# Optimization experiments

Measured on AMD Instinct MI355X. Metric: run time of the kernel, lower is better.

## Reference

```python
import jax, jax.numpy as jnp
import numpy as np

EPS = 1e-5
ROPE_BASE = 10000.0
N_HEAD = 16


def rms_norm(x, eps=EPS):
    return x * jax.lax.rsqrt(jnp.mean(x * x, axis=-1, keepdims=True) + eps)


def rope(x):
    # x: [B, H, L, D]; non-standard interleaved variant from the source:
    # x_odd = x[..., 1::2], x_even = x[..., ::2]
    # y = interleave(y_odd, y_even)
    B, H, L, D = x.shape
    inv_freq = 1.0 / (ROPE_BASE ** (jnp.arange(0, D, 2, dtype=jnp.float32) / D))
    angles = jnp.arange(L, dtype=jnp.float32)[:, None] * inv_freq[None, :]  # [L, D/2]
    cos, sin = jnp.cos(angles), jnp.sin(angles)
    x_odd = x[..., 1::2].astype(jnp.float32)
    x_even = x[..., ::2].astype(jnp.float32)
    y_odd = x_odd * cos - x_even * sin
    y_even = x_odd * sin + x_even * cos
    y = jnp.stack([y_odd, y_even], axis=-1).reshape(B, H, L, D)
    return y.astype(x.dtype)


def setup_inputs() -> dict:
    key = jax.random.key(0)
    k1, k2, k3 = jax.random.split(key, 3)
    B, L, HID = 2, 2048, 2048
    in_std = 0.5 * HID ** (-0.5)
    bound = (3 ** 0.5) * in_std
    x = jax.random.normal(k1, (B, L, HID), dtype=jnp.float32)
    W_qkv = jax.random.uniform(k2, (3 * HID, HID), minval=-bound, maxval=bound, dtype=jnp.float32)
    # out_proj is zero-initialized in the source; use small random weights so the
    # output (and gradients) are non-trivial for correctness checking.
    W_out = jax.random.uniform(k3, (HID, HID), minval=-bound, maxval=bound, dtype=jnp.float32)
    return {"x": x, "W_qkv": W_qkv, "W_out": W_out}


def reference(x, W_qkv, W_out):
    B, L, HID = x.shape
    D = HID // N_HEAD
    qkv = jnp.einsum('blc,fc->blf', x, W_qkv)  # [B, L, 3*HID]
    q, k, v = jnp.split(qkv, 3, axis=-1)
    def heads(t):
        return t.reshape(B, L, N_HEAD, D).transpose(0, 2, 1, 3)  # [B,H,L,D]
    q, k, v = heads(q), heads(k), heads(v)
    q = rope(rms_norm(q))
    k = rope(rms_norm(k))
    scale = 1.0 / jnp.sqrt(jnp.asarray(D, dtype=jnp.float32))
    scores = jnp.einsum('bhqd,bhkd->bhqk', q, k) * scale
    causal = jnp.tril(jnp.ones((L, L), dtype=bool))
    scores = jnp.where(causal, scores, -jnp.inf)
    attn = jax.nn.softmax(scores, axis=-1)
    out = jnp.einsum('bhqk,bhkd->bhqd', attn, v)
    out = out.transpose(0, 2, 1, 3).reshape(B, L, HID)
    return jnp.einsum('blc,fc->blf', out, W_out)
```

## Files before the change

kernel.cpp:

```cpp
#include <hip/hip_runtime.h>
#include <stdint.h>
#include <math.h>

typedef unsigned short u16;
typedef unsigned int u32;
typedef __attribute__((ext_vector_type(8))) short bf16x8;
typedef __attribute__((ext_vector_type(4))) float f32x4;

#define SEQ 2048
#define HID 2048
#define NH  16
#define DH  128
#define NB  2

typedef __attribute__((address_space(1))) const u32 gu32;
typedef __attribute__((address_space(3))) u32 lu32;

__device__ __forceinline__ u16 f2bf(float f) {
  u32 u = __float_as_uint(f);
  return (u16)((u + 0x7fffu + ((u >> 16) & 1u)) >> 16);
}
__device__ __forceinline__ float bf2f(u16 h) { return __uint_as_float(((u32)h) << 16); }

__device__ __forceinline__ void gload_lds16(const void* g, void* l) {
  __builtin_amdgcn_global_load_lds((gu32*)g, (lu32*)l, 16, 0, 0);
}

__global__ __launch_bounds__(256) void k_cvt(const float* __restrict__ src, u16* __restrict__ dst, int n4) {
  int i = blockIdx.x * 256 + threadIdx.x;
  int stride = gridDim.x * 256;
  for (; i < n4; i += stride) {
    float4 v = ((const float4*)src)[i];
    ushort4 o;
    o.x = f2bf(v.x); o.y = f2bf(v.y); o.z = f2bf(v.z); o.w = f2bf(v.w);
    ((ushort4*)dst)[i] = o;
  }
}

template<int EPI>
__global__ __launch_bounds__(256)
void k_gemm(const u16* __restrict__ A, const u16* __restrict__ Bm,
            float* __restrict__ Cf, u16* __restrict__ Qr, u16* __restrict__ Kr, u16* __restrict__ Vr,
            int N, int K, int NX) {
  __shared__ alignas(16) char sA[128 * 128];
  __shared__ alignas(16) char sB[128 * 128];
  const int tid = threadIdx.x;
  const int wid = tid >> 6, lane = tid & 63;
  const int l15 = lane & 15, l4 = lane >> 4;
  const int nwg = gridDim.x, bid = blockIdx.x;
  const int wg = (bid & 7) * (nwg >> 3) + (bid >> 3);
  const int bx = wg % NX, by = wg / NX;
  const int m0 = by * 128, n0 = bx * 128;
  const int wr = (wid >> 1) * 64, wc = (wid & 1) * 64;

  f32x4 acc[4][4];
  #pragma unroll
  for (int i = 0; i < 4; ++i)
    #pragma unroll
    for (int j = 0; j < 4; ++j)
      acc[i][j] = (f32x4){0.f, 0.f, 0.f, 0.f};

  const int nkt = K >> 6;
  for (int kt = 0; kt < nkt; ++kt) {
    const int k0 = kt << 6;
    __syncthreads();
    #pragma unroll
    for (int it = 0; it < 4; ++it) {
      int o = it * 4096 + tid * 16;
      int row = o >> 7, cb = o & 127;
      int scb = cb ^ ((row & 7) << 4);
      gload_lds16((const char*)A + ((size_t)(m0 + row) * K + k0) * 2 + scb, &sA[it * 4096 + wid * 1024]);
    }
    #pragma unroll
    for (int it = 0; it < 4; ++it) {
      int o = it * 4096 + tid * 16;
      int row = o >> 7, cb = o & 127;
      int scb = cb ^ ((row & 7) << 4);
      gload_lds16((const char*)Bm + ((size_t)(n0 + row) * K + k0) * 2 + scb, &sB[it * 4096 + wid * 1024]);
    }
    __syncthreads();
    #pragma unroll
    for (int kk = 0; kk < 2; ++kk) {
      bf16x8 av[4], bv[4];
      #pragma unroll
      for (int mi = 0; mi < 4; ++mi) {
        int row = wr + mi * 16 + l15;
        int colb = kk * 64 + 16 * l4;
        av[mi] = *(const bf16x8*)&sA[row * 128 + (colb ^ ((row & 7) << 4))];
      }
      #pragma unroll
      for (int ni = 0; ni < 4; ++ni) {
        int row = wc + ni * 16 + l15;
        int colb = kk * 64 + 16 * l4;
        bv[ni] = *(const bf16x8*)&sB[row * 128 + (colb ^ ((row & 7) << 4))];
      }
      #pragma unroll
      for (int mi = 0; mi < 4; ++mi)
        #pragma unroll
        for (int ni = 0; ni < 4; ++ni)
          acc[mi][ni] = __builtin_amdgcn_mfma_f32_16x16x32_bf16(av[mi], bv[ni], acc[mi][ni], 0, 0, 0);
    }
  }

  #pragma unroll
  for (int mi = 0; mi < 4; ++mi) {
    #pragma unroll
    for (int ni = 0; ni < 4; ++ni) {
      #pragma unroll
      for (int j = 0; j < 4; ++j) {
        int gm = m0 + wr + mi * 16 + l4 * 4 + j;
        int gn = n0 + wc + ni * 16 + l15;
        float v = acc[mi][ni][j];
        if (EPI == 0) {
          int b = gm >> 11, l = gm & 2047;
          int which = gn >> 11, hid = gn & 2047;
          int h = hid >> 7, d = hid & 127;
          u16* dst = (which == 0) ? Qr : ((which == 1) ? Kr : Vr);
          size_t idx = ((size_t)(b * NH + h) * SEQ + l) * DH + d;
          dst[idx] = f2bf(v);
        } else {
          Cf[(size_t)gm * N + gn] = v;
        }
      }
    }
  }
}

__global__ __launch_bounds__(256) void k_vtr(const u16* __restrict__ Vr, u16* __restrict__ Vt) {
  __shared__ u16 tile[64][72];
  const int k0 = blockIdx.x * 64, d0 = blockIdx.y * 64, bh = blockIdx.z;
  const u16* src = Vr + ((size_t)bh << 18);
  u16* dst = Vt + ((size_t)bh << 18);
  const int tid = threadIdx.x;
  #pragma unroll
  for (int it = 0; it < 2; ++it) {
    int e = it * 2048 + tid * 8;
    int r = e >> 6, c = e & 63;
    bf16x8 v = *(const bf16x8*)(src + (size_t)(k0 + r) * DH + d0 + c);
    *(bf16x8*)&tile[r][c] = v;
  }
  __syncthreads();
  #pragma unroll
  for (int it = 0; it < 2; ++it) {
    int e = it * 2048 + tid * 8;
    int rd = e >> 6, ck = e & 63;
    bf16x8 w;
    #pragma unroll
    for (int i = 0; i < 8; ++i) w[i] = (short)tile[ck + i][rd];
    *(bf16x8*)(dst + (size_t)(d0 + rd) * SEQ + k0 + ck) = w;
  }
}

__global__ __launch_bounds__(256) void k_nrope(u16* __restrict__ T, float mul) {
  const int r = blockIdx.x * 4 + (threadIdx.x >> 6);
  const int lane = threadIdx.x & 63;
  u16* p = T + ((size_t)r << 7) + lane * 2;
  u32 pr = *(const u32*)p;
  float xe = bf2f((u16)(pr & 0xffffu));
  float xo = bf2f((u16)(pr >> 16));
  float ss = xe * xe + xo * xo;
  #pragma unroll
  for (int off = 1; off < 64; off <<= 1) ss += __shfl_xor(ss, off);
  float rinv = rsqrtf(ss * (1.f / 128.f) + 1e-5f);
  float e = xe * rinv, o = xo * rinv;
  int pos = r & (SEQ - 1);
  float freq = exp2f(-0.20762050593046014f * (float)lane);
  float ang = (float)pos * freq;
  float sn, cs;
  sincosf(ang, &sn, &cs);
  u32 outw = (u32)f2bf((o * cs - e * sn) * mul) | ((u32)f2bf((o * sn + e * cs) * mul) << 16);
  *(u32*)p = outw;
}

#define PSTR 72

__device__ __forceinline__ void attn_tile(const char* sK, const char* sVt, char* sPw,
                                          const bf16x8* aq, f32x4* accO, float& m_, float& se,
                                          int qpos, int kb, bool diag, int l15, int l4) {
  f32x4 sacc[4];
  __builtin_amdgcn_s_setprio(1);
  #pragma unroll
  for (int sj = 0; sj < 4; ++sj) {
    sacc[sj] = (f32x4){0.f, 0.f, 0.f, 0.f};
    int row = sj * 16 + l15;
    #pragma unroll
    for (int kk = 0; kk < 4; ++kk) {
      int colb = kk * 64 + 16 * l4;
      bf16x8 bk = *(const bf16x8*)&sK[(row << 8) + (colb ^ ((row & 7) << 4))];
      sacc[sj] = __builtin_amdgcn_mfma_f32_16x16x32_bf16(bk, aq[kk], sacc[sj], 0, 0, 0);
    }
  }
  __builtin_amdgcn_s_setprio(0);
  float pvv[16];
  float mx = -1e30f;
  #pragma unroll
  for (int sj = 0; sj < 4; ++sj)
    #pragma unroll
    for (int j = 0; j < 4; ++j) {
      float s = sacc[sj][j];
      if (diag) {
        int kpos = kb + sj * 16 + l4 * 4 + j;
        s = (kpos > qpos) ? -1e30f : s;
      }
      pvv[sj * 4 + j] = s;
      mx = fmaxf(mx, s);
    }
  mx = fmaxf(mx, __shfl_xor(mx, 16));
  mx = fmaxf(mx, __shfl_xor(mx, 32));
  float mn = fmaxf(m_, mx);
  float corr = __expf(m_ - mn);
  m_ = mn;
  float sum = 0.f;
  #pragma unroll
  for (int i = 0; i < 16; ++i) { float pe = __expf(pvv[i] - mn); pvv[i] = pe; sum += pe; }
  sum += __shfl_xor(sum, 16);
  sum += __shfl_xor(sum, 32);
  se = se * corr + sum;
  float corr4[4];
  #pragma unroll
  for (int j = 0; j < 4; ++j) corr4[j] = __shfl(corr, l4 * 4 + j);
  #pragma unroll
  for (int db = 0; db < 8; ++db) {
    f32x4 a = accO[db];
    #pragma unroll
    for (int j = 0; j < 4; ++j) a[j] *= corr4[j];
    accO[db] = a;
  }
  u16* Pw = (u16*)sPw;
  #pragma unroll
  for (int sj = 0; sj < 4; ++sj)
    #pragma unroll
    for (int jp = 0; jp < 2; ++jp) {
      u32 w = (u32)f2bf(pvv[sj * 4 + jp * 2]) | ((u32)f2bf(pvv[sj * 4 + jp * 2 + 1]) << 16);
      *(u32*)&Pw[l15 * PSTR + sj * 16 + l4 * 4 + jp * 2] = w;
    }
  bf16x8 pa0 = *(const bf16x8*)(sPw + l15 * (PSTR * 2) + 16 * l4);
  bf16x8 pa1 = *(const bf16x8*)(sPw + l15 * (PSTR * 2) + 16 * l4 + 64);
  __builtin_amdgcn_s_setprio(1);
  #pragma unroll
  for (int db = 0; db < 8; ++db) {
    int row = db * 16 + l15;
    const char* vb = &sVt[row * 128];
    bf16x8 b0 = *(const bf16x8*)&vb[(16 * l4) ^ ((row & 7) << 4)];
    bf16x8 b1 = *(const bf16x8*)&vb[(64 + 16 * l4) ^ ((row & 7) << 4)];
    accO[db] = __builtin_amdgcn_mfma_f32_16x16x32_bf16(pa0, b0, accO[db], 0, 0, 0);
    accO[db] = __builtin_amdgcn_mfma_f32_16x16x32_bf16(pa1, b1, accO[db], 0, 0, 0);
  }
  __builtin_amdgcn_s_setprio(0);
}

__device__ __forceinline__ void stage_kv(const char* Kp, const char* Vtp, int kb,
                                         char* bK, char* bV, int tid, int wid) {
  #pragma unroll
  for (int it = 0; it < 4; ++it) {
    int o = it * 4096 + tid * 16;
    int row = o >> 8, cb = o & 255;
    int scb = cb ^ ((row & 7) << 4);
    gload_lds16(Kp + (size_t)(kb + row) * 256 + scb, &bK[it * 4096 + wid * 1024]);
  }
  #pragma unroll
  for (int it = 0; it < 4; ++it) {
    int o = it * 4096 + tid * 16;
    int row = o >> 7, cb = o & 127;
    int scb = cb ^ ((row & 7) << 4);
    gload_lds16(Vtp + (size_t)row * (SEQ * 2) + kb * 2 + scb, &bV[it * 4096 + wid * 1024]);
  }
}

__global__ __launch_bounds__(256, 2)
void k_attn(const u16* __restrict__ Q, const u16* __restrict__ Kg,
            const u16* __restrict__ Vt, u16* __restrict__ O) {
  __shared__ alignas(16) char sK0[64 * 256];
  __shared__ alignas(16) char sK1[64 * 256];
  __shared__ alignas(16) char sV0[128 * 128];
  __shared__ alignas(16) char sV1[128 * 128];
  __shared__ alignas(16) char sP[4 * 16 * PSTR * 2];
  const int tid = threadIdx.x, wid = tid >> 6, lane = tid & 63;
  const int l15 = lane & 15, l4 = lane >> 4;
  const int i = blockIdx.x;
  const int xcd = i & 7, slot = i >> 3;
  const int p = slot & 15;
  const int bh = xcd + 8 * (slot >> 4);
  const int b = bh >> 4, h = bh & 15;
  const int tA = p, tB = 31 - p;
  const u16* Qp = Q + ((size_t)bh << 18);
  const char* Kp = (const char*)(Kg + ((size_t)bh << 18));
  const char* Vtp = (const char*)(Vt + ((size_t)bh << 18));
  const int q0A = tA * 64 + wid * 16;
  const int q0B = tB * 64 + wid * 16;

  bf16x8 aqA[4], aqB[4];
  #pragma unroll
  for (int kk = 0; kk < 4; ++kk) {
    aqA[kk] = *(const bf16x8*)(Qp + (size_t)(q0A + l15) * DH + kk * 32 + 8 * l4);
    aqB[kk] = *(const bf16x8*)(Qp + (size_t)(q0B + l15) * DH + kk * 32 + 8 * l4);
  }

  f32x4 accA[8], accB[8];
  #pragma unroll
  for (int i2 = 0; i2 < 8; ++i2) { accA[i2] = (f32x4){0.f,0.f,0.f,0.f}; accB[i2] = (f32x4){0.f,0.f,0.f,0.f}; }
  float mA = -1e30f, mB = -1e30f, seA = 0.f, seB = 0.f;

  char* sPw = sP + wid * (16 * PSTR * 2);
  const int nt = tB + 1;

  stage_kv(Kp, Vtp, 0, sK0, sV0, tid, wid);
  for (int t = 0; t < nt; ++t) {
    char* bK = (t & 1) ? sK1 : sK0;
    char* bV = (t & 1) ? sV1 : sV0;
    if (t + 1 < nt) {
      stage_kv(Kp, Vtp, (t + 1) << 6, (t & 1) ? sK0 : sK1, (t & 1) ? sV0 : sV1, tid, wid);
      asm volatile("s_waitcnt vmcnt(8)" ::: "memory");
    } else {
      asm volatile("s_waitcnt vmcnt(0)" ::: "memory");
    }
    __builtin_amdgcn_sched_barrier(0);
    __builtin_amdgcn_s_barrier();

    const int kb = t << 6;
    attn_tile(bK, bV, sPw, aqB, accB, mB, seB, q0B + l15, kb, t == tB, l15, l4);
    if (t <= tA)
      attn_tile(bK, bV, sPw, aqA, accA, mA, seA, q0A + l15, kb, t == tA, l15, l4);

    __builtin_amdgcn_s_barrier();
  }

  float seA4[4], seB4[4];
  #pragma unroll
  for (int j = 0; j < 4; ++j) {
    seA4[j] = __shfl(seA, l4 * 4 + j);
    seB4[j] = __shfl(seB, l4 * 4 + j);
  }
  #pragma unroll
  for (int db = 0; db < 8; ++db) {
    #pragma unroll
    for (int j = 0; j < 4; ++j) {
      int d = db * 16 + l15;
      int qA = q0A + l4 * 4 + j;
      int qB = q0B + l4 * 4 + j;
      O[(size_t)(b * SEQ + qA) * HID + h * DH + d] = f2bf(accA[db][j] / seA4[j]);
      O[(size_t)(b * SEQ + qB) * HID + h * DH + d] = f2bf(accB[db][j] / seB4[j]);
    }
  }
}

extern "C" void kernel_launch(void* const* d_in, const int* in_sizes, int n_in,
                              void* d_out, int out_size, void* d_ws, size_t ws_size,
                              hipStream_t stream) {
  (void)in_sizes; (void)n_in; (void)out_size; (void)ws_size;
  const float* x = (const float*)d_in[0];
  const float* Wqkv = (const float*)d_in[1];
  const float* Wout = (const float*)d_in[2];
  float* out = (float*)d_out;
  char* ws = (char*)d_ws;

  u16* xb  = (u16*)(ws);
  u16* wqb = (u16*)(ws + (size_t)16777216);
  u16* Vt  = wqb;
  u16* wob = (u16*)(ws + (size_t)16777216 + 25165824);
  u16* Qr  = (u16*)(ws + (size_t)50331648);
  u16* Kr  = Qr + (size_t)8388608;
  u16* Vr  = Kr + (size_t)8388608;
  u16* Ob  = xb;

  k_cvt<<<dim3(1024), dim3(256), 0, stream>>>(x, xb, (NB * SEQ * HID) / 4);
  k_cvt<<<dim3(1024), dim3(256), 0, stream>>>(Wqkv, wqb, (3 * HID * HID) / 4);
  k_cvt<<<dim3(1024), dim3(256), 0, stream>>>(Wout, wob, (HID * HID) / 4);

  k_gemm<0><<<dim3(1536), dim3(256), 0, stream>>>(xb, wqb, nullptr, Qr, Kr, Vr, 3 * HID, HID, 48);

  k_vtr<<<dim3(SEQ / 64, DH / 64, NB * NH), dim3(256), 0, stream>>>(Vr, Vt);
  k_nrope<<<dim3((NB * NH * SEQ) / 4), dim3(256), 0, stream>>>(Qr, 0.08838834764831845f);
  k_nrope<<<dim3((NB * NH * SEQ) / 4), dim3(256), 0, stream>>>(Kr, 1.0f);

  k_attn<<<dim3(512), dim3(256), 0, stream>>>(Qr, Kr, Vt, Ob);

  k_gemm<1><<<dim3(512), dim3(256), 0, stream>>>(Ob, wob, out, nullptr, nullptr, nullptr, HID, HID, 16);
}
```

Baseline: 301.8 us.

## Merge conversion and rope launches; interleave dual-tile attention with lazy rescale

The three fp32-to-bf16 conversion kernels are merged into one launch, and the two norm+rope launches become a single 2D-grid launch. In attention, the log2(e) factor is folded into the Q scale so exp2 replaces exp. When both query tiles are active, their QK^T and PV MFMAs are interleaved so each K/V fragment is loaded from LDS once. The softmax rescale of the accumulators is skipped unless the running max rises by more than 8, and the P scratch buffer uses an XOR swizzle instead of padding. The aim is fewer launches, less LDS traffic and fewer VALU ops, at the cost of higher register pressure and a threshold-based rescale that trades exactness of the max tracking for fewer multiplies.

After: 298.8 us (median of 3 runs). No clear change (-1.0%).

```diff
diff --git a/kernel.cpp b/kernel.cpp
--- a/kernel.cpp
+++ b/kernel.cpp
@@ -26,14 +26,21 @@
   __builtin_amdgcn_global_load_lds((gu32*)g, (lu32*)l, 16, 0, 0);
 }
 
-__global__ __launch_bounds__(256) void k_cvt(const float* __restrict__ src, u16* __restrict__ dst, int n4) {
+__global__ __launch_bounds__(256) void k_cvt3(const float* __restrict__ s0, u16* __restrict__ d0, int n0,
+                                              const float* __restrict__ s1, u16* __restrict__ d1, int n1,
+                                              const float* __restrict__ s2, u16* __restrict__ d2, int n2) {
   int i = blockIdx.x * 256 + threadIdx.x;
   int stride = gridDim.x * 256;
-  for (; i < n4; i += stride) {
-    float4 v = ((const float4*)src)[i];
+  int total = n0 + n1 + n2;
+  for (; i < total; i += stride) {
+    const float* s; u16* d; int k = i;
+    if (k < n0) { s = s0; d = d0; }
+    else if (k < n0 + n1) { s = s1; d = d1; k -= n0; }
+    else { s = s2; d = d2; k -= n0 + n1; }
+    float4 v = ((const float4*)s)[k];
     ushort4 o;
     o.x = f2bf(v.x); o.y = f2bf(v.y); o.z = f2bf(v.z); o.w = f2bf(v.w);
-    ((ushort4*)dst)[i] = o;
+    ((ushort4*)d)[k] = o;
   }
 }
 
@@ -151,7 +158,9 @@
   }
 }
 
-__global__ __launch_bounds__(256) void k_nrope(u16* __restrict__ T, float mul) {
+__global__ __launch_bounds__(256) void k_nrope2(u16* __restrict__ Qr, u16* __restrict__ Kr, float mq) {
+  u16* T = blockIdx.y ? Kr : Qr;
+  const float mul = blockIdx.y ? 1.0f : mq;
   const int r = blockIdx.x * 4 + (threadIdx.x >> 6);
   const int lane = threadIdx.x & 63;
   u16* p = T + ((size_t)r << 7) + lane * 2;
@@ -172,81 +181,65 @@
   *(u32*)p = outw;
 }
 
-#define PSTR 72
-
-__device__ __forceinline__ void attn_tile(const char* sK, const char* sVt, char* sPw,
-                                          const bf16x8* aq, f32x4* accO, float& m_, float& se,
-                                          int qpos, int kb, bool diag, int l15, int l4) {
-  f32x4 sacc[4];
-  __builtin_amdgcn_s_setprio(1);
-  #pragma unroll
-  for (int sj = 0; sj < 4; ++sj) {
-    sacc[sj] = (f32x4){0.f, 0.f, 0.f, 0.f};
-    int row = sj * 16 + l15;
-    #pragma unroll
-    for (int kk = 0; kk < 4; ++kk) {
-      int colb = kk * 64 + 16 * l4;
-      bf16x8 bk = *(const bf16x8*)&sK[(row << 8) + (colb ^ ((row & 7) << 4))];
-      sacc[sj] = __builtin_amdgcn_mfma_f32_16x16x32_bf16(bk, aq[kk], sacc[sj], 0, 0, 0);
-    }
-  }
-  __builtin_amdgcn_s_setprio(0);
-  float pvv[16];
-  float mx = -1e30f;
+
+__device__ __forceinline__ void smax(f32x4 (&sacc)[4], float& m_, float& se,
+                                     f32x4* accO, u32 (&pw)[8],
+                                     bool diag, int qpos, int kb, int l15, int l4) {
+  if (diag) {
+    #pragma unroll
+    for (int sj = 0; sj < 4; ++sj)
+      #pragma unroll
+      for (int j = 0; j < 4; ++j) {
+        int kpos = kb + sj * 16 + l4 * 4 + j;
+        if (kpos > qpos) sacc[sj][j] = -1e30f;
+      }
+  }
+  float mx = sacc[0][0];
   #pragma unroll
   for (int sj = 0; sj < 4; ++sj)
     #pragma unroll
-    for (int j = 0; j < 4; ++j) {
-      float s = sacc[sj][j];
-      if (diag) {
-        int kpos = kb + sj * 16 + l4 * 4 + j;
-        s = (kpos > qpos) ? -1e30f : s;
-      }
-      pvv[sj * 4 + j] = s;
-      mx = fmaxf(mx, s);
-    }
+    for (int j = 0; j < 4; ++j) mx = fmaxf(mx, sacc[sj][j]);
   mx = fmaxf(mx, __shfl_xor(mx, 16));
   mx = fmaxf(mx, __shfl_xor(mx, 32));
-  float mn = fmaxf(m_, mx);
-  float corr = __expf(m_ - mn);
-  m_ = mn;
+  if (!__all(mx <= m_ + 8.f)) {
+    float mn = fmaxf(m_, mx);
+    float corr = __builtin_exp2f(m_ - mn);
+    m_ = mn;
+    se *= corr;
+    float corr4[4];
+    #pragma unroll
+    for (int j = 0; j < 4; ++j) corr4[j] = __shfl(corr, l4 * 4 + j);
+    #pragma unroll
+    for (int db = 0; db < 8; ++db) {
+      f32x4 a = accO[db];
+      #pragma unroll
+      for (int j = 0; j < 4; ++j) a[j] *= corr4[j];
+      accO[db] = a;
+    }
+  }
   float sum = 0.f;
   #pragma unroll
-  for (int i = 0; i < 16; ++i) { float pe = __expf(pvv[i] - mn); pvv[i] = pe; sum += pe; }
+  for (int sj = 0; sj < 4; ++sj)
+    #pragma unroll
+    for (int jp = 0; jp < 2; ++jp) {
+      float p0 = __builtin_exp2f(sacc[sj][jp * 2]     - m_);
+      float p1 = __builtin_exp2f(sacc[sj][jp * 2 + 1] - m_);
+      pw[sj * 2 + jp] = (u32)f2bf(p0) | ((u32)f2bf(p1) << 16);
+      sum += p0 + p1;
+    }
   sum += __shfl_xor(sum, 16);
   sum += __shfl_xor(sum, 32);
-  se = se * corr + sum;
-  float corr4[4];
-  #pragma unroll
-  for (int j = 0; j < 4; ++j) corr4[j] = __shfl(corr, l4 * 4 + j);
-  #pragma unroll
-  for (int db = 0; db < 8; ++db) {
-    f32x4 a = accO[db];
-    #pragma unroll
-    for (int j = 0; j < 4; ++j) a[j] *= corr4[j];
-    accO[db] = a;
-  }
-  u16* Pw = (u16*)sPw;
+  se += sum;
+}
+
+__device__ __forceinline__ void pwrite(char* sPw, const u32 (&pw)[8], int l15, int l4) {
+  const int sw = (l15 & 7) << 4;
+  char* base = sPw + l15 * 128;
   #pragma unroll
   for (int sj = 0; sj < 4; ++sj)
     #pragma unroll
-    for (int jp = 0; jp < 2; ++jp) {
-      u32 w = (u32)f2bf(pvv[sj * 4 + jp * 2]) | ((u32)f2bf(pvv[sj * 4 + jp * 2 + 1]) << 16);
-      *(u32*)&Pw[l15 * PSTR + sj * 16 + l4 * 4 + jp * 2] = w;
-    }
-  bf16x8 pa0 = *(const bf16x8*)(sPw + l15 * (PSTR * 2) + 16 * l4);
-  bf16x8 pa1 = *(const bf16x8*)(sPw + l15 * (PSTR * 2) + 16 * l4 + 64);
-  __builtin_amdgcn_s_setprio(1);
-  #pragma unroll
-  for (int db = 0; db < 8; ++db) {
-    int row = db * 16 + l15;
-    const char* vb = &sVt[row * 128];
-    bf16x8 b0 = *(const bf16x8*)&vb[(16 * l4) ^ ((row & 7) << 4)];
-    bf16x8 b1 = *(const bf16x8*)&vb[(64 + 16 * l4) ^ ((row & 7) << 4)];
-    accO[db] = __builtin_amdgcn_mfma_f32_16x16x32_bf16(pa0, b0, accO[db], 0, 0, 0);
-    accO[db] = __builtin_amdgcn_mfma_f32_16x16x32_bf16(pa1, b1, accO[db], 0, 0, 0);
-  }
-  __builtin_amdgcn_s_setprio(0);
+    for (int jp = 0; jp < 2; ++jp)
+      *(u32*)(base + ((sj * 32 + l4 * 8 + jp * 4) ^ sw)) = pw[sj * 2 + jp];
 }
 
 __device__ __forceinline__ void stage_kv(const char* Kp, const char* Vtp, int kb,
@@ -274,7 +267,7 @@
   __shared__ alignas(16) char sK1[64 * 256];
   __shared__ alignas(16) char sV0[128 * 128];
   __shared__ alignas(16) char sV1[128 * 128];
-  __shared__ alignas(16) char sP[4 * 16 * PSTR * 2];
+  __shared__ alignas(16) char sP[4 * 2048];
   const int tid = threadIdx.x, wid = tid >> 6, lane = tid & 63;
   const int l15 = lane & 15, l4 = lane >> 4;
   const int i = blockIdx.x;
@@ -301,7 +294,8 @@
   for (int i2 = 0; i2 < 8; ++i2) { accA[i2] = (f32x4){0.f,0.f,0.f,0.f}; accB[i2] = (f32x4){0.f,0.f,0.f,0.f}; }
   float mA = -1e30f, mB = -1e30f, seA = 0.f, seB = 0.f;
 
-  char* sPw = sP + wid * (16 * PSTR * 2);
+  char* sPw = sP + wid * 2048;
+  const int psw = (l15 & 7) << 4;
   const int nt = tB + 1;
 
   stage_kv(Kp, Vtp, 0, sK0, sV0, tid, wid);
@@ -318,9 +312,81 @@
     __builtin_amdgcn_s_barrier();
 
     const int kb = t << 6;
-    attn_tile(bK, bV, sPw, aqB, accB, mB, seB, q0B + l15, kb, t == tB, l15, l4);
-    if (t <= tA)
-      attn_tile(bK, bV, sPw, aqA, accA, mA, seA, q0A + l15, kb, t == tA, l15, l4);
+    if (t <= tA) {
+      f32x4 sb[4], sa[4];
+      __builtin_amdgcn_s_setprio(1);
+      #pragma unroll
+      for (int sj = 0; sj < 4; ++sj) {
+        sb[sj] = (f32x4){0.f,0.f,0.f,0.f};
+        sa[sj] = (f32x4){0.f,0.f,0.f,0.f};
+        int row = sj * 16 + l15;
+        const char* rK = bK + (row << 8);
+        int swr = (row & 7) << 4;
+        #pragma unroll
+        for (int kk = 0; kk < 4; ++kk) {
+          bf16x8 bkv = *(const bf16x8*)(rK + ((kk * 64 + 16 * l4) ^ swr));
+          sb[sj] = __builtin_amdgcn_mfma_f32_16x16x32_bf16(bkv, aqB[kk], sb[sj], 0, 0, 0);
+          sa[sj] = __builtin_amdgcn_mfma_f32_16x16x32_bf16(bkv, aqA[kk], sa[sj], 0, 0, 0);
+        }
+      }
+      __builtin_amdgcn_s_setprio(0);
+      u32 pwB[8], pwA[8];
+      smax(sb, mB, seB, accB, pwB, false, 0, kb, l15, l4);
+      smax(sa, mA, seA, accA, pwA, t == tA, q0A + l15, kb, l15, l4);
+      pwrite(sPw, pwB, l15, l4);
+      bf16x8 paB0 = *(const bf16x8*)(sPw + l15 * 128 + ((16 * l4) ^ psw));
+      bf16x8 paB1 = *(const bf16x8*)(sPw + l15 * 128 + ((64 + 16 * l4) ^ psw));
+      pwrite(sPw, pwA, l15, l4);
+      bf16x8 paA0 = *(const bf16x8*)(sPw + l15 * 128 + ((16 * l4) ^ psw));
+      bf16x8 paA1 = *(const bf16x8*)(sPw + l15 * 128 + ((64 + 16 * l4) ^ psw));
+      __builtin_amdgcn_s_setprio(1);
+      #pragma unroll
+      for (int db = 0; db < 8; ++db) {
+        int row = db * 16 + l15;
+        const char* vb = bV + row * 128;
+        int swr = (row & 7) << 4;
+        bf16x8 b0 = *(const bf16x8*)(vb + ((16 * l4) ^ swr));
+        bf16x8 b1 = *(const bf16x8*)(vb + ((64 + 16 * l4) ^ swr));
+        accB[db] = __builtin_amdgcn_mfma_f32_16x16x32_bf16(paB0, b0, accB[db], 0, 0, 0);
+        accA[db] = __builtin_amdgcn_mfma_f32_16x16x32_bf16(paA0, b0, accA[db], 0, 0, 0);
+        accB[db] = __builtin_amdgcn_mfma_f32_16x16x32_bf16(paB1, b1, accB[db], 0, 0, 0);
+        accA[db] = __builtin_amdgcn_mfma_f32_16x16x32_bf16(paA1, b1, accA[db], 0, 0, 0);
+      }
+      __builtin_amdgcn_s_setprio(0);
+    } else {
+      f32x4 sb[4];
+      __builtin_amdgcn_s_setprio(1);
+      #pragma unroll
+      for (int sj = 0; sj < 4; ++sj) {
+        sb[sj] = (f32x4){0.f,0.f,0.f,0.f};
+        int row = sj * 16 + l15;
+        const char* rK = bK + (row << 8);
+        int swr = (row & 7) << 4;
+        #pragma unroll
+        for (int kk = 0; kk < 4; ++kk) {
+          bf16x8 bkv = *(const bf16x8*)(rK + ((kk * 64 + 16 * l4) ^ swr));
+          sb[sj] = __builtin_amdgcn_mfma_f32_16x16x32_bf16(bkv, aqB[kk], sb[sj], 0, 0, 0);
+        }
+      }
+      __builtin_amdgcn_s_setprio(0);
+      u32 pwB[8];
+      smax(sb, mB, seB, accB, pwB, t == tB, q0B + l15, kb, l15, l4);
+      pwrite(sPw, pwB, l15, l4);
+      bf16x8 paB0 = *(const bf16x8*)(sPw + l15 * 128 + ((16 * l4) ^ psw));
+      bf16x8 paB1 = *(const bf16x8*)(sPw + l15 * 128 + ((64 + 16 * l4) ^ psw));
+      __builtin_amdgcn_s_setprio(1);
+      #pragma unroll
+      for (int db = 0; db < 8; ++db) {
+        int row = db * 16 + l15;
+        const char* vb = bV + row * 128;
+        int swr = (row & 7) << 4;
+        bf16x8 b0 = *(const bf16x8*)(vb + ((16 * l4) ^ swr));
+        bf16x8 b1 = *(const bf16x8*)(vb + ((64 + 16 * l4) ^ swr));
+        accB[db] = __builtin_amdgcn_mfma_f32_16x16x32_bf16(paB0, b0, accB[db], 0, 0, 0);
+        accB[db] = __builtin_amdgcn_mfma_f32_16x16x32_bf16(paB1, b1, accB[db], 0, 0, 0);
+      }
+      __builtin_amdgcn_s_setprio(0);
+    }
 
     __builtin_amdgcn_s_barrier();
   }
@@ -363,15 +429,16 @@
   u16* Vr  = Kr + (size_t)8388608;
   u16* Ob  = xb;
 
-  k_cvt<<<dim3(1024), dim3(256), 0, stream>>>(x, xb, (NB * SEQ * HID) / 4);
-  k_cvt<<<dim3(1024), dim3(256), 0, stream>>>(Wqkv, wqb, (3 * HID * HID) / 4);
-  k_cvt<<<dim3(1024), dim3(256), 0, stream>>>(Wout, wob, (HID * HID) / 4);
+  const float mq = 0.08838834764831845f * 1.4426950408889634f;
+
+  k_cvt3<<<dim3(2048), dim3(256), 0, stream>>>(x, xb, (NB * SEQ * HID) / 4,
+                                               Wqkv, wqb, (3 * HID * HID) / 4,
+                                               Wout, wob, (HID * HID) / 4);
 
   k_gemm<0><<<dim3(1536), dim3(256), 0, stream>>>(xb, wqb, nullptr, Qr, Kr, Vr, 3 * HID, HID, 48);
 
   k_vtr<<<dim3(SEQ / 64, DH / 64, NB * NH), dim3(256), 0, stream>>>(Vr, Vt);
-  k_nrope<<<dim3((NB * NH * SEQ) / 4), dim3(256), 0, stream>>>(Qr, 0.08838834764831845f);
-  k_nrope<<<dim3((NB * NH * SEQ) / 4), dim3(256), 0, stream>>>(Kr, 1.0f);
+  k_nrope2<<<dim3((NB * NH * SEQ) / 4, 2), dim3(256), 0, stream>>>(Qr, Kr, mq);
 
   k_attn<<<dim3(512), dim3(256), 0, stream>>>(Qr, Kr, Vt, Ob);
 
```
